# Kernel optimization log

Hardware: AMD Instinct MI355X
Metric: run time of the kernel (lower is better)

Reference implementation:

```python
import jax, jax.numpy as jnp
import numpy as np

B, T, F, H = 32, 2048, 256, 256  # batch, steps, features, n_hidden
FORGET_BIAS = 1.0  # BasicLSTMCell default


def setup_inputs() -> dict:
    key = jax.random.key(0)
    k1, k2, k3, k4, k5 = jax.random.split(key, 5)
    u = lambda k, shape: jax.random.uniform(k, shape, jnp.float32, -0.1, 0.1)
    return {
        "x": jax.random.normal(k1, (B, T, F), jnp.float32),
        "W_fw": u(k2, (F + H, 4 * H)),  # BasicLSTMCell single kernel [in+hidden, 4H]
        "b_fw": jnp.zeros((4 * H,), jnp.float32),
        "W_bw": u(k3, (F + H, 4 * H)),
        "b_bw": jnp.zeros((4 * H,), jnp.float32),
    }


def _lstm_dir(x, W, b):
    # x: [B,T,F]; W: [F+H,4H]; gate order i, j, f, o (BasicLSTMCell)
    Wx, Wh = W[:F], W[F:]
    xg = jnp.einsum('btf,fg->btg', x, Wx) + b  # precompute input contribution [B,T,4H]

    def step(carry, g_t):
        c, h = carry
        gates = g_t + h @ Wh
        i, j, f, o = jnp.split(gates, 4, axis=-1)
        c = c * jax.nn.sigmoid(f + FORGET_BIAS) + jax.nn.sigmoid(i) * jnp.tanh(j)
        h = jnp.tanh(c) * jax.nn.sigmoid(o)
        return (c, h), h

    init = (jnp.zeros((x.shape[0], H), x.dtype), jnp.zeros((x.shape[0], H), x.dtype))
    _, hs = jax.lax.scan(step, init, jnp.swapaxes(xg, 0, 1))  # [T,B,H]
    return jnp.swapaxes(hs, 0, 1)  # [B,T,H]


def reference(x, W_fw, b_fw, W_bw, b_bw):
    out_fw = _lstm_dir(x, W_fw, b_fw)
    out_bw = _lstm_dir(x[:, ::-1], W_bw, b_bw)[:, ::-1]  # backward direction
    return jnp.concatenate([out_fw, out_bw], axis=-1)  # [B,T,2H]
```

## Files before the change

kernel.cpp:

```cpp
#include <hip/hip_runtime.h>

#define T_LEN 2048

typedef _Float16 f16x8 __attribute__((ext_vector_type(8)));
typedef float f32x4 __attribute__((ext_vector_type(4)));
typedef float f32x2 __attribute__((ext_vector_type(2)));
typedef unsigned long long u64;

__device__ __forceinline__ float sigm(float v) { return 1.f / (1.f + __expf(-v)); }
__device__ __forceinline__ float tanh_f(float v) {
  v = fminf(fmaxf(v, -15.f), 15.f);
  float e = __expf(2.f * v);
  return (e - 1.f) / (e + 1.f);
}

__device__ __forceinline__ void* swzA(_Float16* base, int row, int khalf) {
  int byte = row * 1024 + khalf * 2;
  byte ^= (row & 7) << 4;
  return (void*)((char*)base + byte);
}

__global__ __launch_bounds__(256, 1) void bilstm_kernel(
    const float* __restrict__ x, const float* __restrict__ Wfw,
    const float* __restrict__ bfw, const float* __restrict__ Wbw,
    const float* __restrict__ bbw, float* __restrict__ out,
    u64* __restrict__ hglob) {
  const int g = blockIdx.x & 3;
  const int m = blockIdx.x >> 2;
  const int dir = g >> 1, bh = g & 1;
  const int tid = threadIdx.x;
  const int w = tid >> 6;
  const int lane = tid & 63;
  const int l15 = lane & 15, l4 = lane >> 4;

  const float* W = dir ? Wbw : Wfw;
  const float* bias = dir ? bbw : bfw;

  __shared__ _Float16 Alds[16 * 512];
  __shared__ float Glds[4 * 16 * 34];

  f16x8 wB[2][16];
  {
    const int gc_base = w * 256 + m * 32;
#pragma unroll
    for (int n = 0; n < 2; ++n) {
#pragma unroll
      for (int kk = 0; kk < 16; ++kk) {
        const int gc = gc_base + n * 16 + l15;
        const int kb = kk * 32 + l4 * 8;
        f16x8 h;
#pragma unroll
        for (int j = 0; j < 8; ++j) h[j] = (_Float16)W[(kb + j) * 1024 + gc];
        wB[n][kk] = h;
      }
    }
  }

  const int es = tid >> 4;
  const int ed = (tid & 15) * 2;
  const int dglob = m * 32 + ed;
  float c0 = 0.f, c1 = 0.f;
  const float bi0 = bias[0 * 256 + dglob], bi1 = bias[0 * 256 + dglob + 1];
  const float bj0 = bias[1 * 256 + dglob], bj1 = bias[1 * 256 + dglob + 1];
  const float bf0 = bias[2 * 256 + dglob], bf1 = bias[2 * 256 + dglob + 1];
  const float bo0 = bias[3 * 256 + dglob], bo1 = bias[3 * 256 + dglob + 1];

  const int ss = tid >> 4;
  const int sk = (tid & 15) * 16;

  u64* Hg = hglob + (u64)g * (2 * 16 * 128);
  u64* my_slot0 = Hg + (0 * 16 + es) * 128 + (dglob >> 1);
  u64* my_slot1 = Hg + (1 * 16 + es) * 128 + (dglob >> 1);

  {
    uint4 z = {0u, 0u, 0u, 0u};
    *(uint4*)swzA(Alds, ss, 256 + sk) = z;
    *(uint4*)swzA(Alds, ss, 256 + sk + 8) = z;
  }
  const int tx0 = dir ? (T_LEN - 1) : 0;
  const f32x4* xp0 = (const f32x4*)(x + (((bh * 16 + ss) * T_LEN + tx0) << 8) + sk);
  f32x4 xv0 = xp0[0], xv1 = xp0[1], xv2 = xp0[2], xv3 = xp0[3];

  for (int t = 0; t < T_LEN; ++t) {
    const int tx = dir ? (T_LEN - 1 - t) : t;

    {
      union { _Float16 h[16]; uint4 q[2]; } u;
#pragma unroll
      for (int j = 0; j < 4; ++j) {
        u.h[j] = (_Float16)xv0[j];
        u.h[4 + j] = (_Float16)xv1[j];
        u.h[8 + j] = (_Float16)xv2[j];
        u.h[12 + j] = (_Float16)xv3[j];
      }
      *(uint4*)swzA(Alds, ss, sk) = u.q[0];
      *(uint4*)swzA(Alds, ss, sk + 8) = u.q[1];
    }
    __syncthreads();

    {
      const int tn = (t + 1 < T_LEN) ? t + 1 : t;
      const int txn = dir ? (T_LEN - 1 - tn) : tn;
      const f32x4* xp =
          (const f32x4*)(x + (((bh * 16 + ss) * T_LEN + txn) << 8) + sk);
      xv0 = xp[0]; xv1 = xp[1]; xv2 = xp[2]; xv3 = xp[3];
    }

    f32x4 acc0 = {0.f, 0.f, 0.f, 0.f}, acc1 = {0.f, 0.f, 0.f, 0.f};
#pragma unroll
    for (int kk = 0; kk < 8; ++kk) {
      f16x8 a = *(const f16x8*)swzA(Alds, l15, kk * 32 + l4 * 8);
      acc0 = __builtin_amdgcn_mfma_f32_16x16x32_f16(a, wB[0][kk], acc0, 0, 0, 0);
      acc1 = __builtin_amdgcn_mfma_f32_16x16x32_f16(a, wB[1][kk], acc1, 0, 0, 0);
    }

    if (t > 0) {
      const u64* hp = Hg + (((t - 1) & 1) * 16 + ss) * 128 + (sk >> 1);
      u64 q[8];
      for (;;) {
#pragma unroll
        for (int j = 0; j < 8; ++j)
          q[j] = __hip_atomic_load(hp + j, __ATOMIC_RELAXED,
                                   __HIP_MEMORY_SCOPE_AGENT);
        bool ok = true;
#pragma unroll
        for (int j = 0; j < 8; ++j)
          ok &= ((unsigned int)(q[j] >> 32) == (unsigned int)t);
        if (__all(ok)) break;
      }
      uint4 q0 = {(unsigned)q[0], (unsigned)q[1], (unsigned)q[2], (unsigned)q[3]};
      uint4 q1 = {(unsigned)q[4], (unsigned)q[5], (unsigned)q[6], (unsigned)q[7]};
      *(uint4*)swzA(Alds, ss, 256 + sk) = q0;
      *(uint4*)swzA(Alds, ss, 256 + sk + 8) = q1;
    }
    __syncthreads();

#pragma unroll
    for (int kk = 8; kk < 16; ++kk) {
      f16x8 a = *(const f16x8*)swzA(Alds, l15, kk * 32 + l4 * 8);
      acc0 = __builtin_amdgcn_mfma_f32_16x16x32_f16(a, wB[0][kk], acc0, 0, 0, 0);
      acc1 = __builtin_amdgcn_mfma_f32_16x16x32_f16(a, wB[1][kk], acc1, 0, 0, 0);
    }

    {
      float* gw = Glds + w * 544 + l15;
      const int r = l4 * 4;
#pragma unroll
      for (int v = 0; v < 4; ++v) {
        gw[(r + v) * 34] = acc0[v];
        gw[(r + v) * 34 + 16] = acc1[v];
      }
    }
    __syncthreads();

    const float* Gp = Glds + es * 34 + ed;
    f32x2 gi = *(const f32x2*)(Gp + 0 * 544);
    f32x2 gj = *(const f32x2*)(Gp + 1 * 544);
    f32x2 gf = *(const f32x2*)(Gp + 2 * 544);
    f32x2 go = *(const f32x2*)(Gp + 3 * 544);
    c0 = c0 * sigm(gf[0] + bf0 + 1.f) + sigm(gi[0] + bi0) * tanh_f(gj[0] + bj0);
    c1 = c1 * sigm(gf[1] + bf1 + 1.f) + sigm(gi[1] + bi1) * tanh_f(gj[1] + bj1);
    float h0 = tanh_f(c0) * sigm(go[0] + bo0);
    float h1 = tanh_f(c1) * sigm(go[1] + bo1);

    union { _Float16 hh[2]; unsigned int u; } pk;
    pk.hh[0] = (_Float16)h0;
    pk.hh[1] = (_Float16)h1;
    u64 pay = ((u64)(unsigned int)(t + 1) << 32) | (u64)pk.u;
    __hip_atomic_store((t & 1) ? my_slot1 : my_slot0, pay, __ATOMIC_RELAXED,
                       __HIP_MEMORY_SCOPE_AGENT);

    f32x2 hv = {h0, h1};
    __builtin_nontemporal_store(
        hv, (f32x2*)(out + (((bh * 16 + es) * T_LEN + tx) << 9) + dir * 256 + dglob));
  }
}

extern "C" void kernel_launch(void* const* d_in, const int* in_sizes, int n_in,
                              void* d_out, int out_size, void* d_ws,
                              size_t ws_size, hipStream_t stream) {
  const float* x = (const float*)d_in[0];
  const float* Wfw = (const float*)d_in[1];
  const float* bfw = (const float*)d_in[2];
  const float* Wbw = (const float*)d_in[3];
  const float* bbw = (const float*)d_in[4];
  float* out = (float*)d_out;

  u64* hglob = (u64*)d_ws;
  (void)hipMemsetAsync(hglob, 0, 4 * 2 * 16 * 128 * sizeof(u64), stream);

  bilstm_kernel<<<dim3(32), dim3(256), 0, stream>>>(x, Wfw, bfw, Wbw, bbw, out,
                                                    hglob);
}
```

Measured before the change: 4.955 ms.

## Compute LSTM gates in MFMA registers and pack h with 16-bit stamps

Remaps weight columns so each wave's MFMA output pairs the i/f and j/o gates across lanes. Gate math then runs directly on accumulator registers using lane shuffles, which removes the Glds round-trip and one __syncthreads per step. Bias is folded into the accumulator init, and tanh is computed through sigmoid. The h exchange switches to 32-bit words holding a 16-bit step stamp and an fp16 value, with the first poll issued before the MFMAs and double-buffered polling loads. Risks are the 16-bit stamp wrap (2048 steps fit) and more, smaller atomic loads per thread.

```diff
diff --git a/kernel.cpp b/kernel.cpp
--- a/kernel.cpp
+++ b/kernel.cpp
@@ -4,15 +4,9 @@
 
 typedef _Float16 f16x8 __attribute__((ext_vector_type(8)));
 typedef float f32x4 __attribute__((ext_vector_type(4)));
-typedef float f32x2 __attribute__((ext_vector_type(2)));
-typedef unsigned long long u64;
+typedef unsigned int u32;
 
 __device__ __forceinline__ float sigm(float v) { return 1.f / (1.f + __expf(-v)); }
-__device__ __forceinline__ float tanh_f(float v) {
-  v = fminf(fmaxf(v, -15.f), 15.f);
-  float e = __expf(2.f * v);
-  return (e - 1.f) / (e + 1.f);
-}
 
 __device__ __forceinline__ void* swzA(_Float16* base, int row, int khalf) {
   int byte = row * 1024 + khalf * 2;
@@ -24,7 +18,7 @@
     const float* __restrict__ x, const float* __restrict__ Wfw,
     const float* __restrict__ bfw, const float* __restrict__ Wbw,
     const float* __restrict__ bbw, float* __restrict__ out,
-    u64* __restrict__ hglob) {
+    u32* __restrict__ hglob) {
   const int g = blockIdx.x & 3;
   const int m = blockIdx.x >> 2;
   const int dir = g >> 1, bh = g & 1;
@@ -32,148 +26,177 @@
   const int w = tid >> 6;
   const int lane = tid & 63;
   const int l15 = lane & 15, l4 = lane >> 4;
+  const bool lo8 = (l15 < 8);
+  const int d8 = l15 & 7;
+  const int mw8 = m * 32 + w * 8;
 
   const float* W = dir ? Wbw : Wfw;
   const float* bias = dir ? bbw : bfw;
 
   __shared__ _Float16 Alds[16 * 512];
-  __shared__ float Glds[4 * 16 * 34];
-
-  f16x8 wB[2][16];
-  {
-    const int gc_base = w * 256 + m * 32;
-#pragma unroll
-    for (int n = 0; n < 2; ++n) {
-#pragma unroll
-      for (int kk = 0; kk < 16; ++kk) {
-        const int gc = gc_base + n * 16 + l15;
-        const int kb = kk * 32 + l4 * 8;
-        f16x8 h;
-#pragma unroll
-        for (int j = 0; j < 8; ++j) h[j] = (_Float16)W[(kb + j) * 1024 + gc];
-        wB[n][kk] = h;
-      }
-    }
-  }
-
-  const int es = tid >> 4;
-  const int ed = (tid & 15) * 2;
-  const int dglob = m * 32 + ed;
-  float c0 = 0.f, c1 = 0.f;
-  const float bi0 = bias[0 * 256 + dglob], bi1 = bias[0 * 256 + dglob + 1];
-  const float bj0 = bias[1 * 256 + dglob], bj1 = bias[1 * 256 + dglob + 1];
-  const float bf0 = bias[2 * 256 + dglob], bf1 = bias[2 * 256 + dglob + 1];
-  const float bo0 = bias[3 * 256 + dglob], bo1 = bias[3 * 256 + dglob + 1];
+
+  const int gc0 = (lo8 ? 0 : 512) + mw8 + d8;
+  const int gc1 = (lo8 ? 256 : 768) + mw8 + d8;
+
+  f16x8 wB0[16], wB1[16];
+#pragma unroll
+  for (int kk = 0; kk < 16; ++kk) {
+    const int kb = kk * 32 + l4 * 8;
+    f16x8 h0, h1;
+#pragma unroll
+    for (int j = 0; j < 8; ++j) {
+      h0[j] = (_Float16)W[(kb + j) * 1024 + gc0];
+      h1[j] = (_Float16)W[(kb + j) * 1024 + gc1];
+    }
+    wB0[kk] = h0;
+    wB1[kk] = h1;
+  }
+  const float b0 = bias[gc0] + (lo8 ? 0.f : 1.f);
+  const float b1 = bias[gc1];
 
   const int ss = tid >> 4;
-  const int sk = (tid & 15) * 16;
-
-  u64* Hg = hglob + (u64)g * (2 * 16 * 128);
-  u64* my_slot0 = Hg + (0 * 16 + es) * 128 + (dglob >> 1);
-  u64* my_slot1 = Hg + (1 * 16 + es) * 128 + (dglob >> 1);
+  const int si = tid & 15;
+  const int dA = 8 * si, dB = 128 + 8 * si;
+
+  u32* Hg = hglob + g * (2 * 16 * 256);
+
+  float c[4] = {0.f, 0.f, 0.f, 0.f};
 
   {
     uint4 z = {0u, 0u, 0u, 0u};
-    *(uint4*)swzA(Alds, ss, 256 + sk) = z;
-    *(uint4*)swzA(Alds, ss, 256 + sk + 8) = z;
+    *(uint4*)swzA(Alds, ss, 256 + dA) = z;
+    *(uint4*)swzA(Alds, ss, 256 + dB) = z;
   }
   const int tx0 = dir ? (T_LEN - 1) : 0;
-  const f32x4* xp0 = (const f32x4*)(x + (((bh * 16 + ss) * T_LEN + tx0) << 8) + sk);
-  f32x4 xv0 = xp0[0], xv1 = xp0[1], xv2 = xp0[2], xv3 = xp0[3];
+  const float* xr0 = x + (((bh * 16 + ss) * T_LEN + tx0) << 8);
+  f32x4 xa0 = *(const f32x4*)(xr0 + dA);
+  f32x4 xa1 = *(const f32x4*)(xr0 + dA + 4);
+  f32x4 xb0 = *(const f32x4*)(xr0 + dB);
+  f32x4 xb1 = *(const f32x4*)(xr0 + dB + 4);
+
+#define LOADQ(q)                                                              \
+  {                                                                           \
+    _Pragma("unroll") for (int j_ = 0; j_ < 8; ++j_) q[j_] =                  \
+        __hip_atomic_load(hp + dA + j_, __ATOMIC_RELAXED,                     \
+                          __HIP_MEMORY_SCOPE_AGENT);                          \
+    _Pragma("unroll") for (int j_ = 0; j_ < 8; ++j_) q[8 + j_] =              \
+        __hip_atomic_load(hp + dB + j_, __ATOMIC_RELAXED,                     \
+                          __HIP_MEMORY_SCOPE_AGENT);                          \
+  }
+#define CHECKQ(q, okv)                                                        \
+  {                                                                           \
+    bool ok_ = true;                                                          \
+    _Pragma("unroll") for (int j_ = 0; j_ < 16; ++j_) ok_ &=                  \
+        ((q[j_] >> 16) == want);                                              \
+    okv = ok_;                                                                \
+  }
 
   for (int t = 0; t < T_LEN; ++t) {
     const int tx = dir ? (T_LEN - 1 - t) : t;
 
     {
-      union { _Float16 h[16]; uint4 q[2]; } u;
+      union { _Float16 h[8]; uint4 q; } ua, ub;
 #pragma unroll
       for (int j = 0; j < 4; ++j) {
-        u.h[j] = (_Float16)xv0[j];
-        u.h[4 + j] = (_Float16)xv1[j];
-        u.h[8 + j] = (_Float16)xv2[j];
-        u.h[12 + j] = (_Float16)xv3[j];
+        ua.h[j] = (_Float16)xa0[j];
+        ua.h[4 + j] = (_Float16)xa1[j];
+        ub.h[j] = (_Float16)xb0[j];
+        ub.h[4 + j] = (_Float16)xb1[j];
       }
-      *(uint4*)swzA(Alds, ss, sk) = u.q[0];
-      *(uint4*)swzA(Alds, ss, sk + 8) = u.q[1];
+      *(uint4*)swzA(Alds, ss, dA) = ua.q;
+      *(uint4*)swzA(Alds, ss, dB) = ub.q;
     }
     __syncthreads();
 
     {
       const int tn = (t + 1 < T_LEN) ? t + 1 : t;
       const int txn = dir ? (T_LEN - 1 - tn) : tn;
-      const f32x4* xp =
-          (const f32x4*)(x + (((bh * 16 + ss) * T_LEN + txn) << 8) + sk);
-      xv0 = xp[0]; xv1 = xp[1]; xv2 = xp[2]; xv3 = xp[3];
-    }
-
-    f32x4 acc0 = {0.f, 0.f, 0.f, 0.f}, acc1 = {0.f, 0.f, 0.f, 0.f};
+      const float* xr = x + (((bh * 16 + ss) * T_LEN + txn) << 8);
+      xa0 = *(const f32x4*)(xr + dA);
+      xa1 = *(const f32x4*)(xr + dA + 4);
+      xb0 = *(const f32x4*)(xr + dB);
+      xb1 = *(const f32x4*)(xr + dB + 4);
+    }
+
+    u32 qA[16], qB[16];
+    const u32* hp = Hg + (((t - 1) & 1) * 16 + ss) * 256;
+    const u32 want = (u32)t;
+    if (t > 0) LOADQ(qA);
+
+    f32x4 acc0 = {b0, b0, b0, b0}, acc1 = {b1, b1, b1, b1};
 #pragma unroll
     for (int kk = 0; kk < 8; ++kk) {
       f16x8 a = *(const f16x8*)swzA(Alds, l15, kk * 32 + l4 * 8);
-      acc0 = __builtin_amdgcn_mfma_f32_16x16x32_f16(a, wB[0][kk], acc0, 0, 0, 0);
-      acc1 = __builtin_amdgcn_mfma_f32_16x16x32_f16(a, wB[1][kk], acc1, 0, 0, 0);
+      acc0 = __builtin_amdgcn_mfma_f32_16x16x32_f16(a, wB0[kk], acc0, 0, 0, 0);
+      acc1 = __builtin_amdgcn_mfma_f32_16x16x32_f16(a, wB1[kk], acc1, 0, 0, 0);
     }
 
     if (t > 0) {
-      const u64* hp = Hg + (((t - 1) & 1) * 16 + ss) * 128 + (sk >> 1);
-      u64 q[8];
-      for (;;) {
-#pragma unroll
-        for (int j = 0; j < 8; ++j)
-          q[j] = __hip_atomic_load(hp + j, __ATOMIC_RELAXED,
-                                   __HIP_MEMORY_SCOPE_AGENT);
-        bool ok = true;
-#pragma unroll
-        for (int j = 0; j < 8; ++j)
-          ok &= ((unsigned int)(q[j] >> 32) == (unsigned int)t);
-        if (__all(ok)) break;
+      bool ok;
+      CHECKQ(qA, ok);
+      if (!ok) {
+        LOADQ(qB);
+        for (;;) {
+          LOADQ(qA);
+          CHECKQ(qB, ok);
+          if (ok) {
+#pragma unroll
+            for (int j = 0; j < 16; ++j) qA[j] = qB[j];
+            break;
+          }
+          LOADQ(qB);
+          CHECKQ(qA, ok);
+          if (ok) break;
+        }
       }
-      uint4 q0 = {(unsigned)q[0], (unsigned)q[1], (unsigned)q[2], (unsigned)q[3]};
-      uint4 q1 = {(unsigned)q[4], (unsigned)q[5], (unsigned)q[6], (unsigned)q[7]};
-      *(uint4*)swzA(Alds, ss, 256 + sk) = q0;
-      *(uint4*)swzA(Alds, ss, 256 + sk + 8) = q1;
+      uint4 pa, pb;
+      pa.x = (qA[0] & 0xffffu) | (qA[1] << 16);
+      pa.y = (qA[2] & 0xffffu) | (qA[3] << 16);
+      pa.z = (qA[4] & 0xffffu) | (qA[5] << 16);
+      pa.w = (qA[6] & 0xffffu) | (qA[7] << 16);
+      pb.x = (qA[8] & 0xffffu) | (qA[9] << 16);
+      pb.y = (qA[10] & 0xffffu) | (qA[11] << 16);
+      pb.z = (qA[12] & 0xffffu) | (qA[13] << 16);
+      pb.w = (qA[14] & 0xffffu) | (qA[15] << 16);
+      *(uint4*)swzA(Alds, ss, 256 + dA) = pa;
+      *(uint4*)swzA(Alds, ss, 256 + dB) = pb;
     }
     __syncthreads();
 
 #pragma unroll
     for (int kk = 8; kk < 16; ++kk) {
       f16x8 a = *(const f16x8*)swzA(Alds, l15, kk * 32 + l4 * 8);
-      acc0 = __builtin_amdgcn_mfma_f32_16x16x32_f16(a, wB[0][kk], acc0, 0, 0, 0);
-      acc1 = __builtin_amdgcn_mfma_f32_16x16x32_f16(a, wB[1][kk], acc1, 0, 0, 0);
-    }
-
-    {
-      float* gw = Glds + w * 544 + l15;
-      const int r = l4 * 4;
-#pragma unroll
-      for (int v = 0; v < 4; ++v) {
-        gw[(r + v) * 34] = acc0[v];
-        gw[(r + v) * 34 + 16] = acc1[v];
+      acc0 = __builtin_amdgcn_mfma_f32_16x16x32_f16(a, wB0[kk], acc0, 0, 0, 0);
+      acc1 = __builtin_amdgcn_mfma_f32_16x16x32_f16(a, wB1[kk], acc1, 0, 0, 0);
+    }
+
+    const u32 stamp = ((u32)(t + 1)) << 16;
+    u32* pub = Hg + ((t & 1) * 16) * 256 + mw8 + d8;
+#pragma unroll
+    for (int v = 0; v < 4; ++v) {
+      float s0 = sigm(acc0[v]);
+      float a1v = acc1[v];
+      float uu = lo8 ? a1v + a1v : a1v;
+      float s1 = sigm(uu);
+      float g1 = lo8 ? 2.f * s1 - 1.f : s1;
+      float sf = __shfl_xor(s0, 8);
+      float so = __shfl_xor(g1, 8);
+      c[v] = c[v] * sf + s0 * g1;
+      float tc = 2.f * sigm(c[v] + c[v]) - 1.f;
+      float h = tc * so;
+      if (lo8) {
+        union { _Float16 hf; unsigned short us; } cv;
+        cv.hf = (_Float16)h;
+        const int seq = 4 * l4 + v;
+        __hip_atomic_store(pub + seq * 256, stamp | (u32)cv.us,
+                           __ATOMIC_RELAXED, __HIP_MEMORY_SCOPE_AGENT);
+        __builtin_nontemporal_store(
+            h, out + (((bh * 16 + seq) * T_LEN + tx) << 9) + dir * 256 + mw8 + d8);
       }
     }
-    __syncthreads();
-
-    const float* Gp = Glds + es * 34 + ed;
-    f32x2 gi = *(const f32x2*)(Gp + 0 * 544);
-    f32x2 gj = *(const f32x2*)(Gp + 1 * 544);
-    f32x2 gf = *(const f32x2*)(Gp + 2 * 544);
-    f32x2 go = *(const f32x2*)(Gp + 3 * 544);
-    c0 = c0 * sigm(gf[0] + bf0 + 1.f) + sigm(gi[0] + bi0) * tanh_f(gj[0] + bj0);
-    c1 = c1 * sigm(gf[1] + bf1 + 1.f) + sigm(gi[1] + bi1) * tanh_f(gj[1] + bj1);
-    float h0 = tanh_f(c0) * sigm(go[0] + bo0);
-    float h1 = tanh_f(c1) * sigm(go[1] + bo1);
-
-    union { _Float16 hh[2]; unsigned int u; } pk;
-    pk.hh[0] = (_Float16)h0;
-    pk.hh[1] = (_Float16)h1;
-    u64 pay = ((u64)(unsigned int)(t + 1) << 32) | (u64)pk.u;
-    __hip_atomic_store((t & 1) ? my_slot1 : my_slot0, pay, __ATOMIC_RELAXED,
-                       __HIP_MEMORY_SCOPE_AGENT);
-
-    f32x2 hv = {h0, h1};
-    __builtin_nontemporal_store(
-        hv, (f32x2*)(out + (((bh * 16 + es) * T_LEN + tx) << 9) + dir * 256 + dglob));
-  }
+  }
+#undef LOADQ
+#undef CHECKQ
 }
 
 extern "C" void kernel_launch(void* const* d_in, const int* in_sizes, int n_in,
@@ -186,8 +209,8 @@
   const float* bbw = (const float*)d_in[4];
   float* out = (float*)d_out;
 
-  u64* hglob = (u64*)d_ws;
-  (void)hipMemsetAsync(hglob, 0, 4 * 2 * 16 * 128 * sizeof(u64), stream);
+  u32* hglob = (u32*)d_ws;
+  (void)hipMemsetAsync(hglob, 0, 4 * 2 * 16 * 256 * sizeof(u32), stream);
 
   bilstm_kernel<<<dim3(32), dim3(256), 0, stream>>>(x, Wfw, bfw, Wbw, bbw, out,
                                                     hglob);
```

Result: slower. 7.103 ms (+43.3%).

## Repartition LSTM across 16 blocks of 1024 threads with 32-bit tagged h exchange

Applied to the files above, without the earlier changes.

Changes the work split from 32 blocks of 256 threads (8 per direction/batch-half group) to 16 blocks of 1024 threads (4 per group). Each block now owns 64 hidden units, and each of its 16 waves computes one 16-column MFMA tile. The cross-block h exchange uses packed 32-bit words (16-bit step tag plus fp16 value), and each block writes its own slice straight into LDS, so fewer peers are polled each step. Bias is folded into the accumulator init and tanh is computed via sigmoid. The intent is to cut inter-block synchronization and polling traffic per step, at the cost of fewer CUs in use and a larger per-block barrier.

```diff
diff --git a/kernel.cpp b/kernel.cpp
--- a/kernel.cpp
+++ b/kernel.cpp
@@ -4,27 +4,21 @@
 
 typedef _Float16 f16x8 __attribute__((ext_vector_type(8)));
 typedef float f32x4 __attribute__((ext_vector_type(4)));
-typedef float f32x2 __attribute__((ext_vector_type(2)));
-typedef unsigned long long u64;
+typedef unsigned int u32;
 
 __device__ __forceinline__ float sigm(float v) { return 1.f / (1.f + __expf(-v)); }
-__device__ __forceinline__ float tanh_f(float v) {
-  v = fminf(fmaxf(v, -15.f), 15.f);
-  float e = __expf(2.f * v);
-  return (e - 1.f) / (e + 1.f);
-}
 
-__device__ __forceinline__ void* swzA(_Float16* base, int row, int khalf) {
-  int byte = row * 1024 + khalf * 2;
+__device__ __forceinline__ void* swzA(_Float16* base, int row, int k) {
+  int byte = row * 1024 + k * 2;
   byte ^= (row & 7) << 4;
   return (void*)((char*)base + byte);
 }
 
-__global__ __launch_bounds__(256, 1) void bilstm_kernel(
+__global__ __launch_bounds__(1024, 4) void bilstm_kernel(
     const float* __restrict__ x, const float* __restrict__ Wfw,
     const float* __restrict__ bfw, const float* __restrict__ Wbw,
     const float* __restrict__ bbw, float* __restrict__ out,
-    u64* __restrict__ hglob) {
+    u32* __restrict__ hglob) {
   const int g = blockIdx.x & 3;
   const int m = blockIdx.x >> 2;
   const int dir = g >> 1, bh = g & 1;
@@ -37,142 +31,111 @@
   const float* bias = dir ? bbw : bfw;
 
   __shared__ _Float16 Alds[16 * 512];
-  __shared__ float Glds[4 * 16 * 34];
+  __shared__ float Glds[16 * 260];
 
-  f16x8 wB[2][16];
-  {
-    const int gc_base = w * 256 + m * 32;
+  const int p = w >> 2;
+  const int cbase = p * 64 + (w & 3) * 16;
+  const int gcol = p * 256 + 64 * m + (w & 3) * 16 + l15;
+  f16x8 wB[16];
 #pragma unroll
-    for (int n = 0; n < 2; ++n) {
+  for (int kk = 0; kk < 16; ++kk) {
+    const int kb = kk * 32 + l4 * 8;
+    f16x8 h;
 #pragma unroll
-      for (int kk = 0; kk < 16; ++kk) {
-        const int gc = gc_base + n * 16 + l15;
-        const int kb = kk * 32 + l4 * 8;
-        f16x8 h;
-#pragma unroll
-        for (int j = 0; j < 8; ++j) h[j] = (_Float16)W[(kb + j) * 1024 + gc];
-        wB[n][kk] = h;
-      }
-    }
+    for (int j = 0; j < 8; ++j) h[j] = (_Float16)W[(kb + j) * 1024 + gcol];
+    wB[kk] = h;
   }
+  const float bcol = bias[gcol] + ((p == 2) ? 1.f : 0.f);
 
-  const int es = tid >> 4;
-  const int ed = (tid & 15) * 2;
-  const int dglob = m * 32 + ed;
-  float c0 = 0.f, c1 = 0.f;
-  const float bi0 = bias[0 * 256 + dglob], bi1 = bias[0 * 256 + dglob + 1];
-  const float bj0 = bias[1 * 256 + dglob], bj1 = bias[1 * 256 + dglob + 1];
-  const float bf0 = bias[2 * 256 + dglob], bf1 = bias[2 * 256 + dglob + 1];
-  const float bo0 = bias[3 * 256 + dglob], bo1 = bias[3 * 256 + dglob + 1];
+  const int cs = tid >> 6;
+  const int cd = tid & 63;
+  float c = 0.f;
 
-  const int ss = tid >> 4;
-  const int sk = (tid & 15) * 16;
-
-  u64* Hg = hglob + (u64)g * (2 * 16 * 128);
-  u64* my_slot0 = Hg + (0 * 16 + es) * 128 + (dglob >> 1);
-  u64* my_slot1 = Hg + (1 * 16 + es) * 128 + (dglob >> 1);
+  u32* Hg = hglob + g * (2 * 16 * 256);
+  const int pd1 = 64 * ((m + 1) & 3) + cd;
+  const int pd2 = 64 * ((m + 2) & 3) + cd;
+  const int pd3 = 64 * ((m + 3) & 3) + cd;
+  u32* mypub[2] = {Hg + (0 * 16 + cs) * 256 + 64 * m + cd,
+                   Hg + (1 * 16 + cs) * 256 + 64 * m + cd};
 
   {
-    uint4 z = {0u, 0u, 0u, 0u};
-    *(uint4*)swzA(Alds, ss, 256 + sk) = z;
-    *(uint4*)swzA(Alds, ss, 256 + sk + 8) = z;
+    uint2 z = {0u, 0u};
+    *(uint2*)swzA(Alds, cs, 256 + 4 * cd) = z;
   }
   const int tx0 = dir ? (T_LEN - 1) : 0;
-  const f32x4* xp0 = (const f32x4*)(x + (((bh * 16 + ss) * T_LEN + tx0) << 8) + sk);
-  f32x4 xv0 = xp0[0], xv1 = xp0[1], xv2 = xp0[2], xv3 = xp0[3];
+  f32x4 xv = *(const f32x4*)(x + (((bh * 16 + cs) * T_LEN + tx0) << 8) + 4 * cd);
 
   for (int t = 0; t < T_LEN; ++t) {
     const int tx = dir ? (T_LEN - 1 - t) : t;
 
     {
-      union { _Float16 h[16]; uint4 q[2]; } u;
+      union { _Float16 h[4]; uint2 q; } ux;
 #pragma unroll
-      for (int j = 0; j < 4; ++j) {
-        u.h[j] = (_Float16)xv0[j];
-        u.h[4 + j] = (_Float16)xv1[j];
-        u.h[8 + j] = (_Float16)xv2[j];
-        u.h[12 + j] = (_Float16)xv3[j];
-      }
-      *(uint4*)swzA(Alds, ss, sk) = u.q[0];
-      *(uint4*)swzA(Alds, ss, sk + 8) = u.q[1];
+      for (int j = 0; j < 4; ++j) ux.h[j] = (_Float16)xv[j];
+      *(uint2*)swzA(Alds, cs, 4 * cd) = ux.q;
     }
     __syncthreads();
+
+    const u32 want = (u32)t;
+    const u32* Hp = Hg + (((t & 1) ^ 1) * 16 + cs) * 256;
+    u32 s1 = 0, s2 = 0, s3 = 0;
+    if (t > 0) {
+      s1 = __hip_atomic_load(Hp + pd1, __ATOMIC_RELAXED, __HIP_MEMORY_SCOPE_AGENT);
+      s2 = __hip_atomic_load(Hp + pd2, __ATOMIC_RELAXED, __HIP_MEMORY_SCOPE_AGENT);
+      s3 = __hip_atomic_load(Hp + pd3, __ATOMIC_RELAXED, __HIP_MEMORY_SCOPE_AGENT);
+    }
 
     {
       const int tn = (t + 1 < T_LEN) ? t + 1 : t;
       const int txn = dir ? (T_LEN - 1 - tn) : tn;
-      const f32x4* xp =
-          (const f32x4*)(x + (((bh * 16 + ss) * T_LEN + txn) << 8) + sk);
-      xv0 = xp[0]; xv1 = xp[1]; xv2 = xp[2]; xv3 = xp[3];
+      xv = *(const f32x4*)(x + (((bh * 16 + cs) * T_LEN + txn) << 8) + 4 * cd);
     }
 
-    f32x4 acc0 = {0.f, 0.f, 0.f, 0.f}, acc1 = {0.f, 0.f, 0.f, 0.f};
+    f32x4 acc = {bcol, bcol, bcol, bcol};
 #pragma unroll
     for (int kk = 0; kk < 8; ++kk) {
       f16x8 a = *(const f16x8*)swzA(Alds, l15, kk * 32 + l4 * 8);
-      acc0 = __builtin_amdgcn_mfma_f32_16x16x32_f16(a, wB[0][kk], acc0, 0, 0, 0);
-      acc1 = __builtin_amdgcn_mfma_f32_16x16x32_f16(a, wB[1][kk], acc1, 0, 0, 0);
+      acc = __builtin_amdgcn_mfma_f32_16x16x32_f16(a, wB[kk], acc, 0, 0, 0);
     }
 
     if (t > 0) {
-      const u64* hp = Hg + (((t - 1) & 1) * 16 + ss) * 128 + (sk >> 1);
-      u64 q[8];
-      for (;;) {
-#pragma unroll
-        for (int j = 0; j < 8; ++j)
-          q[j] = __hip_atomic_load(hp + j, __ATOMIC_RELAXED,
-                                   __HIP_MEMORY_SCOPE_AGENT);
-        bool ok = true;
-#pragma unroll
-        for (int j = 0; j < 8; ++j)
-          ok &= ((unsigned int)(q[j] >> 32) == (unsigned int)t);
-        if (__all(ok)) break;
+      while ((s1 >> 16) != want || (s2 >> 16) != want || (s3 >> 16) != want) {
+        s1 = __hip_atomic_load(Hp + pd1, __ATOMIC_RELAXED, __HIP_MEMORY_SCOPE_AGENT);
+        s2 = __hip_atomic_load(Hp + pd2, __ATOMIC_RELAXED, __HIP_MEMORY_SCOPE_AGENT);
+        s3 = __hip_atomic_load(Hp + pd3, __ATOMIC_RELAXED, __HIP_MEMORY_SCOPE_AGENT);
       }
-      uint4 q0 = {(unsigned)q[0], (unsigned)q[1], (unsigned)q[2], (unsigned)q[3]};
-      uint4 q1 = {(unsigned)q[4], (unsigned)q[5], (unsigned)q[6], (unsigned)q[7]};
-      *(uint4*)swzA(Alds, ss, 256 + sk) = q0;
-      *(uint4*)swzA(Alds, ss, 256 + sk + 8) = q1;
+      *(unsigned short*)swzA(Alds, cs, 256 + pd1) = (unsigned short)(s1 & 0xffffu);
+      *(unsigned short*)swzA(Alds, cs, 256 + pd2) = (unsigned short)(s2 & 0xffffu);
+      *(unsigned short*)swzA(Alds, cs, 256 + pd3) = (unsigned short)(s3 & 0xffffu);
     }
     __syncthreads();
 
 #pragma unroll
     for (int kk = 8; kk < 16; ++kk) {
       f16x8 a = *(const f16x8*)swzA(Alds, l15, kk * 32 + l4 * 8);
-      acc0 = __builtin_amdgcn_mfma_f32_16x16x32_f16(a, wB[0][kk], acc0, 0, 0, 0);
-      acc1 = __builtin_amdgcn_mfma_f32_16x16x32_f16(a, wB[1][kk], acc1, 0, 0, 0);
+      acc = __builtin_amdgcn_mfma_f32_16x16x32_f16(a, wB[kk], acc, 0, 0, 0);
     }
 
     {
-      float* gw = Glds + w * 544 + l15;
+      float* gw = Glds + cbase + l15;
       const int r = l4 * 4;
 #pragma unroll
-      for (int v = 0; v < 4; ++v) {
-        gw[(r + v) * 34] = acc0[v];
-        gw[(r + v) * 34 + 16] = acc1[v];
-      }
+      for (int v = 0; v < 4; ++v) gw[(r + v) * 260] = acc[v];
     }
     __syncthreads();
 
-    const float* Gp = Glds + es * 34 + ed;
-    f32x2 gi = *(const f32x2*)(Gp + 0 * 544);
-    f32x2 gj = *(const f32x2*)(Gp + 1 * 544);
-    f32x2 gf = *(const f32x2*)(Gp + 2 * 544);
-    f32x2 go = *(const f32x2*)(Gp + 3 * 544);
-    c0 = c0 * sigm(gf[0] + bf0 + 1.f) + sigm(gi[0] + bi0) * tanh_f(gj[0] + bj0);
-    c1 = c1 * sigm(gf[1] + bf1 + 1.f) + sigm(gi[1] + bi1) * tanh_f(gj[1] + bj1);
-    float h0 = tanh_f(c0) * sigm(go[0] + bo0);
-    float h1 = tanh_f(c1) * sigm(go[1] + bo1);
+    const float* Gp = Glds + cs * 260 + cd;
+    const float gi = Gp[0 * 64], gj = Gp[1 * 64], gf = Gp[2 * 64], go = Gp[3 * 64];
+    c = c * sigm(gf) + sigm(gi) * (2.f * sigm(gj + gj) - 1.f);
+    const float h = (2.f * sigm(c + c) - 1.f) * sigm(go);
 
-    union { _Float16 hh[2]; unsigned int u; } pk;
-    pk.hh[0] = (_Float16)h0;
-    pk.hh[1] = (_Float16)h1;
-    u64 pay = ((u64)(unsigned int)(t + 1) << 32) | (u64)pk.u;
-    __hip_atomic_store((t & 1) ? my_slot1 : my_slot0, pay, __ATOMIC_RELAXED,
-                       __HIP_MEMORY_SCOPE_AGENT);
-
-    f32x2 hv = {h0, h1};
+    union { _Float16 hf; unsigned short us; } cv;
+    cv.hf = (_Float16)h;
+    __hip_atomic_store(mypub[t & 1], (((u32)(t + 1)) << 16) | (u32)cv.us,
+                       __ATOMIC_RELAXED, __HIP_MEMORY_SCOPE_AGENT);
+    *(unsigned short*)swzA(Alds, cs, 256 + 64 * m + cd) = cv.us;
     __builtin_nontemporal_store(
-        hv, (f32x2*)(out + (((bh * 16 + es) * T_LEN + tx) << 9) + dir * 256 + dglob));
+        h, out + (((bh * 16 + cs) * T_LEN + tx) << 9) + dir * 256 + 64 * m + cd);
   }
 }
 
@@ -186,9 +149,9 @@
   const float* bbw = (const float*)d_in[4];
   float* out = (float*)d_out;
 
-  u64* hglob = (u64*)d_ws;
-  (void)hipMemsetAsync(hglob, 0, 4 * 2 * 16 * 128 * sizeof(u64), stream);
+  u32* hglob = (u32*)d_ws;
+  (void)hipMemsetAsync(hglob, 0, 4 * 2 * 16 * 256 * sizeof(u32), stream);
 
-  bilstm_kernel<<<dim3(32), dim3(256), 0, stream>>>(x, Wfw, bfw, Wbw, bbw, out,
-                                                    hglob);
+  bilstm_kernel<<<dim3(16), dim3(1024), 0, stream>>>(x, Wfw, bfw, Wbw, bbw, out,
+                                                     hglob);
 }
```

Result: faster. 4.826 ms (-2.6%).
